# Kernel optimization log

Hardware: AMD Instinct MI355X
Metric: run time of the kernel (lower is better)

Reference implementation:

```python
import jax, jax.numpy as jnp
import numpy as np

B, L = 1, 320
CS, CZ, CH, H, PQ, PV = 384, 128, 16, 12, 4, 8
INF, EPS = 1e5, 1e-8


def _quat_to_rot(q):
    w, x, y, z = q[..., 0], q[..., 1], q[..., 2], q[..., 3]
    r0 = jnp.stack([1 - 2*(y*y + z*z), 2*(x*y - w*z), 2*(x*z + w*y)], -1)
    r1 = jnp.stack([2*(x*y + w*z), 1 - 2*(x*x + z*z), 2*(y*z - w*x)], -1)
    r2 = jnp.stack([2*(x*z - w*y), 2*(y*z + w*x), 1 - 2*(x*x + y*y)], -1)
    return jnp.stack([r0, r1, r2], -2)


def setup_inputs():
    key = jax.random.key(0)
    ks = jax.random.split(key, 12)

    def lin(k, fan_in, fan_out):
        k1, k2 = jax.random.split(k)
        lim = 1.0 / np.sqrt(fan_in)
        return (jax.random.uniform(k1, (fan_in, fan_out), minval=-lim, maxval=lim, dtype=jnp.float32),
                jax.random.uniform(k2, (fan_out,), minval=-lim, maxval=lim, dtype=jnp.float32))

    s = jax.random.normal(ks[0], (B, L, CS), dtype=jnp.float32)
    quat = jax.random.normal(ks[1], (B, L, 4), dtype=jnp.float32)
    quat = quat / jnp.linalg.norm(quat, axis=-1, keepdims=True)
    rot = _quat_to_rot(quat)                                   # proper rotations (B,L,3,3)
    trans = 10.0 * jax.random.normal(ks[2], (B, L, 3), dtype=jnp.float32)
    z = jax.random.normal(ks[3], (B, L, L, CZ), dtype=jnp.float32)
    frame_mask = jnp.ones((B, L), dtype=jnp.float32)

    Wq, bq = lin(ks[4], CS, CH * H)
    Wkv, bkv = lin(ks[5], CS, 2 * CH * H)
    Wqp, bqp = lin(ks[6], CS, 6 * H * PQ)
    Wkvp, bkvp = lin(ks[7], CS, 6 * H * (PQ + PV))
    Wg, bg = lin(ks[8], CS, H * PQ)
    geom_weights = jnp.ones((3,), jnp.float32)
    dir_weight = jnp.asarray(0.5, jnp.float32)
    head_weights = 0.02 * jax.random.normal(ks[9], (H,), dtype=jnp.float32)
    concat_dim = H * (CH + 7 * PV) + H * CZ                    # 2400
    Wo, bo = lin(ks[10], concat_dim, CS)
    return dict(s=s, rot=rot, trans=trans, z=z, frame_mask=frame_mask,
                Wq=Wq, bq=bq, Wkv=Wkv, bkv=bkv, Wqp=Wqp, bqp=bqp,
                Wkvp=Wkvp, bkvp=bkvp, Wg=Wg, bg=bg,
                geom_weights=geom_weights, dir_weight=dir_weight,
                head_weights=head_weights, Wo=Wo, bo=bo)


def reference(s, rot, trans, z, frame_mask, Wq, bq, Wkv, bkv, Wqp, bqp,
              Wkvp, bkvp, Wg, bg, geom_weights, dir_weight, head_weights, Wo, bo):
    def proc_pts(pts_flat, P):
        # (B,L,6*H*P) -> rotate coords+translate, rotate dirs -> (B,L,H,P,6)
        pts = pts_flat.reshape(B, L, H, P, 6)
        coords = jnp.einsum('blij,blhpj->blhpi', rot, pts[..., :3]) + trans[:, :, None, None, :]
        dirs = jnp.einsum('blij,blhpj->blhpi', rot, pts[..., 3:])
        return jnp.concatenate([coords, dirs], -1)

    q = (s @ Wq + bq).reshape(B, L, H, CH)
    kv = s @ Wkv + bkv
    k = kv[..., :CH * H].reshape(B, L, H, CH)
    v = kv[..., CH * H:].reshape(B, L, H, CH)

    q_pts = proc_pts(s @ Wqp + bqp, PQ)
    kv_pts = s @ Wkvp + bkvp
    k_pts = proc_pts(kv_pts[..., :6 * H * PQ], PQ)
    v_pts = proc_pts(kv_pts[..., 6 * H * PQ:], PV)

    gate = jax.nn.sigmoid(s @ Wg + bg).reshape(B, L, H, PQ, 1)
    q_pts = q_pts * gate

    scalar_att = jnp.einsum('bqhc,bkhc->bhqk', q, k) / np.sqrt(CH).astype(np.float32)

    # position attention: per-pair point distances + log + inverse, mean over points
    delta = q_pts[:, :, None, :, :, :3] - k_pts[:, None, :, :, :, :3]   # (B,Lq,Lk,H,PQ,3)
    d = jnp.linalg.norm(delta, axis=-1)
    pos_att = (d + jnp.log(d + EPS) + 1.0 / (d + EPS)).mean(-1).transpose(0, 3, 1, 2)

    # direction attention: per-point dot minus cross-product 'curvature'
    qd, kd = q_pts[..., 3:], k_pts[..., 3:]
    dot = jnp.einsum('bqhpd,bkhpd->bqkhp', qd, kd)                       # (B,Lq,Lk,H,P)
    cr = jnp.cross(qd[:, :, None, :, None, :, :], kd[:, None, :, :, :, None, :])  # (B,Lq,Lk,H,Pk,Pq,3)
    cross = jnp.linalg.norm(cr, axis=-1).mean(-1)                        # (B,Lq,Lk,H,Pk)
    nq = jnp.linalg.norm(qd, axis=-1)[:, :, None]                        # (B,Lq,1,H,P)
    nk = jnp.linalg.norm(kd, axis=-1)[:, None]                           # (B,1,Lk,H,P)
    dir_att = (dot - cross / (nq * nk + EPS)).mean(-1).transpose(0, 3, 1, 2)

    att = scalar_att + dir_weight * (geom_weights[0] * pos_att + geom_weights[1] * dir_att)
    att = att * head_weights[:, None, None]
    mask2d = frame_mask[:, None, None, :] * frame_mask[:, None, :, None]  # (B,1,L,L)
    att = jax.nn.softmax(att + INF * (mask2d - 1.0), axis=-1)

    o_scalar = jnp.einsum('bhqk,bkhc->bqhc', att, v)
    o_geom = jnp.einsum('bhqk,bkhpd->bqhpd', att, v_pts)                 # (B,L,H,PV,6)

    # map aggregated geometry back into local frames
    rotT = jnp.swapaxes(rot, -1, -2)
    trans_inv = -jnp.einsum('blij,blj->bli', rotT, trans)
    lc = jnp.einsum('blij,blhpj->blhpi', rotT, o_geom[..., :3]) + trans_inv[:, :, None, None, :]
    ld = jnp.einsum('blij,blhpj->blhpi', rotT, o_geom[..., 3:6])
    ld = ld / jnp.maximum(jnp.linalg.norm(ld, axis=-1, keepdims=True), 1e-12)  # F.normalize
    ln = jnp.linalg.norm(lc, axis=-1, keepdims=True)
    o_geom7 = jnp.concatenate([lc, ld, ln], -1)                          # (B,L,H,PV,7)

    o_pair = jnp.einsum('bhij,bijk->bihk', att, z)                       # (B,L,H,CZ)
    out = jnp.concatenate([o_scalar.reshape(B, L, H * CH),
                           o_geom7.reshape(B, L, H * PV * 7),
                           o_pair.reshape(B, L, H * CZ)], -1)
    return out @ Wo + bo
```

## Files before the change

kernel.cpp:

```cpp
#include <hip/hip_runtime.h>
#include <hip/hip_bf16.h>
#include <math.h>

#define LSEQ 320
#define CS 384
#define CZ 128
#define CH 16
#define NH 12
#define PQ 4
#define PV 8
#define EPSF 1e-8f

typedef short short8 __attribute__((ext_vector_type(8)));
typedef float f32x4 __attribute__((ext_vector_type(4)));

__device__ __forceinline__ unsigned short f2b(float x) {
    union { float f; unsigned u; } v; v.f = x;
    unsigned r = (v.u + 0x7FFF + ((v.u >> 16) & 1)) >> 16;
    return (unsigned short)r;
}
__device__ __forceinline__ float b2f(unsigned short h) {
    union { unsigned u; float f; } v; v.u = ((unsigned)h) << 16;
    return v.f;
}

#define OFF_Q      0
#define OFF_KV     61440
#define OFF_QPT    184320
#define OFF_KPT    276480
#define OFF_OG     368640
#define OFF_ATTHI  552960
#define OFF_ATTLO  1372160
#define OFF_CCHI   2191360
#define OFF_CCLO   2575360
#define OFF_SHI    2959360
#define OFF_SLO    2990080
#define OFF_WCATHI 3020800
#define OFF_WCATLO 3361792
#define OFF_BCAT   3702784
#define OFF_WOHI   3704560
#define OFF_WOLO   4165360
#define OFF_VKVHI  4626160
#define OFF_VKVLO  4749040
#define OFF_QPR    4871920
#define OFF_KVPR   4964080
#define OFF_GATE   5240560

__global__ __launch_bounds__(256) void k_cast(
    const float* __restrict__ s,
    const float* __restrict__ Wq, const float* __restrict__ bq,
    const float* __restrict__ Wkv, const float* __restrict__ bkv,
    const float* __restrict__ Wqp, const float* __restrict__ bqp,
    const float* __restrict__ Wkvp, const float* __restrict__ bkvp,
    const float* __restrict__ Wg, const float* __restrict__ bg,
    const float* __restrict__ Wo,
    unsigned short* __restrict__ s_hi, unsigned short* __restrict__ s_lo,
    unsigned short* __restrict__ wcat_hi, unsigned short* __restrict__ wcat_lo,
    float* __restrict__ bcat,
    unsigned short* __restrict__ wo_hi, unsigned short* __restrict__ wo_lo)
{
    int i = blockIdx.x * 256 + threadIdx.x;
    if (i < 122880) {
        float x = s[i];
        unsigned short hi = f2b(x);
        s_hi[i] = hi; s_lo[i] = f2b(x - b2f(hi));
        return;
    }
    i -= 122880;
    if (i < 681984) {
        int k = i / 1776, c = i - k * 1776;
        float v;
        if (c < 192)       v = Wq[(size_t)k * 192 + c];
        else if (c < 576)  v = Wkv[(size_t)k * 384 + c - 192];
        else if (c < 864)  v = Wqp[(size_t)k * 288 + c - 576];
        else if (c < 1728) v = Wkvp[(size_t)k * 864 + c - 864];
        else               v = Wg[(size_t)k * 48 + c - 1728];
        unsigned short hi = f2b(v);
        wcat_hi[i] = hi; wcat_lo[i] = f2b(v - b2f(hi));
        return;
    }
    i -= 681984;
    if (i < 1776) {
        float v;
        if (i < 192)       v = bq[i];
        else if (i < 576)  v = bkv[i - 192];
        else if (i < 864)  v = bqp[i - 576];
        else if (i < 1728) v = bkvp[i - 864];
        else               v = bg[i - 1728];
        bcat[i] = v;
        return;
    }
    i -= 1776;
    if (i < 921600) {
        float v = Wo[i];
        unsigned short hi = f2b(v);
        wo_hi[i] = hi; wo_lo[i] = f2b(v - b2f(hi));
    }
}

__global__ __launch_bounds__(256) void k_proj(
    const unsigned short* __restrict__ s_hi, const unsigned short* __restrict__ s_lo,
    const unsigned short* __restrict__ wcat_hi, const unsigned short* __restrict__ wcat_lo,
    const float* __restrict__ bcat,
    float* __restrict__ qo, float* __restrict__ kvo,
    float* __restrict__ qpr, float* __restrict__ kvpr, float* __restrict__ gate)
{
    __shared__ unsigned short a_hi[64][56];
    __shared__ unsigned short a_lo[64][56];
    __shared__ unsigned short w_hi[48][56];
    __shared__ unsigned short w_lo[48][56];
    int col0 = blockIdx.x * 48, l0 = blockIdx.y * 64;
    int tid = threadIdx.x;
    int lane = tid & 63, w = tid >> 6;
    int ncol = lane & 15, blk = lane >> 4, mrow = (lane >> 4) * 4;

    float* dst; int nc, cbase; bool sig = false;
    if (col0 < 192)       { nc = 192; cbase = col0;        dst = qo;   }
    else if (col0 < 576)  { nc = 384; cbase = col0 - 192;  dst = kvo;  }
    else if (col0 < 864)  { nc = 288; cbase = col0 - 576;  dst = qpr;  }
    else if (col0 < 1728) { nc = 864; cbase = col0 - 864;  dst = kvpr; }
    else                  { nc = 48;  cbase = 0;           dst = gate; sig = true; }

    f32x4 acc[3] = {};
    for (int k0 = 0; k0 < 384; k0 += 32) {
        __syncthreads();
        {
            int row = tid >> 2, seg = tid & 3;
            size_t off = (size_t)(l0 + row) * 384 + k0 + seg * 8;
            *(short8*)&a_hi[row][seg * 8] = *(const short8*)(s_hi + off);
            *(short8*)&a_lo[row][seg * 8] = *(const short8*)(s_lo + off);
        }
        if (tid < 96) {
            int kk = tid / 3, coff = (tid % 3) * 16;
            size_t off = (size_t)(k0 + kk) * 1776 + col0 + coff;
            short8 h0 = *(const short8*)(wcat_hi + off);
            short8 h1 = *(const short8*)(wcat_hi + off + 8);
            short8 l0v = *(const short8*)(wcat_lo + off);
            short8 l1v = *(const short8*)(wcat_lo + off + 8);
            #pragma unroll
            for (int i = 0; i < 8; i++) {
                w_hi[coff + i][kk]     = (unsigned short)h0[i];
                w_hi[coff + 8 + i][kk] = (unsigned short)h1[i];
                w_lo[coff + i][kk]     = (unsigned short)l0v[i];
                w_lo[coff + 8 + i][kk] = (unsigned short)l1v[i];
            }
        }
        __syncthreads();
        short8 afh = *(short8*)&a_hi[w * 16 + ncol][blk * 8];
        short8 afl = *(short8*)&a_lo[w * 16 + ncol][blk * 8];
        #pragma unroll
        for (int s3 = 0; s3 < 3; s3++) {
            short8 bfh = *(short8*)&w_hi[s3 * 16 + ncol][blk * 8];
            short8 bfl = *(short8*)&w_lo[s3 * 16 + ncol][blk * 8];
            acc[s3] = __builtin_amdgcn_mfma_f32_16x16x32_bf16(afh, bfh, acc[s3], 0, 0, 0);
            acc[s3] = __builtin_amdgcn_mfma_f32_16x16x32_bf16(afh, bfl, acc[s3], 0, 0, 0);
            acc[s3] = __builtin_amdgcn_mfma_f32_16x16x32_bf16(afl, bfh, acc[s3], 0, 0, 0);
        }
    }
    #pragma unroll
    for (int s3 = 0; s3 < 3; s3++) {
        float bv = bcat[col0 + s3 * 16 + ncol];
        int cloc = cbase + s3 * 16 + ncol;
        #pragma unroll
        for (int r = 0; r < 4; r++) {
            float v2 = acc[s3][r] + bv;
            if (sig) v2 = 1.0f / (1.0f + expf(-v2));
            dst[(size_t)(l0 + w * 16 + mrow + r) * nc + cloc] = v2;
        }
    }
}

__global__ __launch_bounds__(256) void k_points(
    const float* __restrict__ qpr, const float* __restrict__ kvpr, const float* __restrict__ gate,
    const float* __restrict__ rot, const float* __restrict__ trans,
    const float* __restrict__ kv,
    float* __restrict__ qpt, float* __restrict__ kpt,
    unsigned short* __restrict__ vkv_hi, unsigned short* __restrict__ vkv_lo)
{
    __shared__ float vsh[96][6];
    int l = blockIdx.x, t = threadIdx.x;
    const float* R = rot + l * 9;
    float tx = trans[l * 3], ty = trans[l * 3 + 1], tz = trans[l * 3 + 2];
    if (t < 192) {
        const float* src; float g = 1.0f; float* dst = nullptr; int vj = -1;
        if (t < 48)      { src = qpr + (size_t)l * 288 + t * 6; g = gate[l * 48 + t]; dst = qpt + ((size_t)l * 48 + t) * 6; }
        else if (t < 96) { int j = t - 48; src = kvpr + (size_t)l * 864 + j * 6; dst = kpt + ((size_t)l * 48 + j) * 6; }
        else             { int j = t - 96; src = kvpr + (size_t)l * 864 + 288 + j * 6; vj = j; }
        float px = src[0], py = src[1], pz = src[2], ux = src[3], uy = src[4], uz = src[5];
        float c0 = R[0] * px + R[1] * py + R[2] * pz + tx;
        float c1 = R[3] * px + R[4] * py + R[5] * pz + ty;
        float c2 = R[6] * px + R[7] * py + R[8] * pz + tz;
        float d0 = R[0] * ux + R[1] * uy + R[2] * uz;
        float d1 = R[3] * ux + R[4] * uy + R[5] * uz;
        float d2 = R[6] * ux + R[7] * uy + R[8] * uz;
        if (vj >= 0) {
            vsh[vj][0] = c0; vsh[vj][1] = c1; vsh[vj][2] = c2;
            vsh[vj][3] = d0; vsh[vj][4] = d1; vsh[vj][5] = d2;
        } else {
            dst[0] = c0 * g; dst[1] = c1 * g; dst[2] = c2 * g;
            dst[3] = d0 * g; dst[4] = d1 * g; dst[5] = d2 * g;
        }
    }
    __syncthreads();
    #pragma unroll
    for (int e = 0; e < 3; e++) {
        int u = t * 3 + e;
        int h = u >> 6, n = u & 63;
        float val;
        if (n < 16) val = kv[(size_t)l * 384 + 192 + h * 16 + n];
        else        val = vsh[h * 8 + (n - 16) / 6][(n - 16) % 6];
        unsigned short hi = f2b(val);
        size_t idx = ((size_t)h * 64 + n) * 320 + l;
        vkv_hi[idx] = hi;
        vkv_lo[idx] = f2b(val - b2f(hi));
    }
}

__global__ __launch_bounds__(256) void k_att(
    const float* __restrict__ qb, const float* __restrict__ kvb,
    const float* __restrict__ qpt, const float* __restrict__ kpt,
    const float* __restrict__ fm, const float* __restrict__ gw,
    const float* __restrict__ dwp, const float* __restrict__ hwp,
    unsigned short* __restrict__ att_hi, unsigned short* __restrict__ att_lo)
{
    __shared__ float kp_sh[320][25];
    int tid = threadIdx.x;
    int w = tid >> 6, lane = tid & 63;
    int iq = blockIdx.x * 4 + w;
    int h = blockIdx.y;

    for (int idx = tid; idx < 7680; idx += 256) {
        int kk = idx / 24, j = idx - kk * 24;
        kp_sh[kk][j] = kpt[(size_t)kk * 288 + h * 24 + j];
    }
    __syncthreads();

    float qv[CH];
    #pragma unroll
    for (int c = 0; c < CH; c++) qv[c] = qb[(size_t)iq * 192 + h * CH + c];
    float qp[24];
    #pragma unroll
    for (int j = 0; j < 24; j++) qp[j] = qpt[(size_t)iq * 288 + h * 24 + j];
    float nq[PQ];
    #pragma unroll
    for (int p = 0; p < PQ; p++) {
        float x = qp[p * 6 + 3], y = qp[p * 6 + 4], zz = qp[p * 6 + 5];
        nq[p] = sqrtf(x * x + y * y + zz * zz);
    }
    float dwv = dwp[0], g0 = gw[0], g1 = gw[1], hwv = hwp[h];
    float fmi = fm[iq];

    float lg[5];
    #pragma unroll
    for (int r = 0; r < 5; r++) {
        int kk = r * 64 + lane;
        const float* kp = &kp_sh[kk][0];

        float scalar = 0.f;
        #pragma unroll
        for (int c = 0; c < CH; c++) scalar += qv[c] * kvb[(size_t)kk * 384 + h * CH + c];
        scalar *= 0.25f;

        float pos = 0.f;
        #pragma unroll
        for (int p = 0; p < PQ; p++) {
            float dx = qp[p * 6] - kp[p * 6], dy = qp[p * 6 + 1] - kp[p * 6 + 1], dz = qp[p * 6 + 2] - kp[p * 6 + 2];
            float d = sqrtf(dx * dx + dy * dy + dz * dz);
            pos += d + logf(d + EPSF) + 1.0f / (d + EPSF);
        }
        pos *= 0.25f;

        float dir = 0.f;
        #pragma unroll
        for (int p = 0; p < PQ; p++) {
            float kx = kp[p * 6 + 3], ky = kp[p * 6 + 4], kz = kp[p * 6 + 5];
            float nk = sqrtf(kx * kx + ky * ky + kz * kz);
            float cm = 0.f;
            #pragma unroll
            for (int pq = 0; pq < PQ; pq++) {
                float qx = qp[pq * 6 + 3], qy = qp[pq * 6 + 4], qz = qp[pq * 6 + 5];
                float cx = qy * kz - qz * ky;
                float cy = qz * kx - qx * kz;
                float cz = qx * ky - qy * kx;
                cm += sqrtf(cx * cx + cy * cy + cz * cz);
            }
            cm *= 0.25f;
            float qx = qp[p * 6 + 3], qy = qp[p * 6 + 4], qz = qp[p * 6 + 5];
            float dotp = qx * kx + qy * ky + qz * kz;
            dir += dotp - cm / (nq[p] * nk + EPSF);
        }
        dir *= 0.25f;

        float logit = scalar + dwv * (g0 * pos + g1 * dir);
        logit *= hwv;
        logit += 100000.0f * (fmi * fm[kk] - 1.0f);
        lg[r] = logit;
    }

    float mx = lg[0];
    #pragma unroll
    for (int r = 1; r < 5; r++) mx = fmaxf(mx, lg[r]);
    for (int m = 32; m; m >>= 1) mx = fmaxf(mx, __shfl_xor(mx, m, 64));

    float e[5], sm = 0.f;
    #pragma unroll
    for (int r = 0; r < 5; r++) { e[r] = expf(lg[r] - mx); sm += e[r]; }
    for (int m = 32; m; m >>= 1) sm += __shfl_xor(sm, m, 64);
    float inv = 1.0f / sm;
    #pragma unroll
    for (int r = 0; r < 5; r++) {
        float p = e[r] * inv;
        unsigned short hi = f2b(p);
        size_t idx = ((size_t)h * 320 + iq) * 320 + r * 64 + lane;
        att_hi[idx] = hi;
        att_lo[idx] = f2b(p - b2f(hi));
    }
}

__global__ __launch_bounds__(256) void k_initzero(
    const float* __restrict__ bo, float* __restrict__ out,
    float* __restrict__ ph_hi, float* __restrict__ ph_lo)
{
    int i = blockIdx.x * 256 + threadIdx.x;
    if (i < 204800) ph_hi[i] = 0.0f;
    else if (i < 409600) ph_lo[i - 204800] = 0.0f;
    else { int j = i - 409600; out[j] = bo[j % CS]; }
}

__global__ __launch_bounds__(64) void k_sv(
    const unsigned short* __restrict__ att_hi, const unsigned short* __restrict__ att_lo,
    const unsigned short* __restrict__ vkv_hi, const unsigned short* __restrict__ vkv_lo,
    unsigned short* __restrict__ cc_hi, unsigned short* __restrict__ cc_lo,
    float* __restrict__ og)
{
    __shared__ unsigned short a_hi[16][56];
    __shared__ unsigned short a_lo[16][56];
    __shared__ unsigned short bt_hi[64][56];
    __shared__ unsigned short bt_lo[64][56];
    int iq0 = blockIdx.x * 16, h = blockIdx.y;
    int tid = threadIdx.x;
    int ncol = tid & 15, blk = tid >> 4, mrow = (tid >> 4) * 4;

    f32x4 acc[4] = {};
    for (int k0 = 0; k0 < 320; k0 += 32) {
        __syncthreads();
        {
            int row = tid >> 2, seg = tid & 3;
            size_t off = ((size_t)h * 320 + iq0 + row) * 320 + k0 + seg * 8;
            *(short8*)&a_hi[row][seg * 8] = *(const short8*)(att_hi + off);
            *(short8*)&a_lo[row][seg * 8] = *(const short8*)(att_lo + off);
        }
        {
            size_t off = ((size_t)h * 64 + tid) * 320 + k0;
            #pragma unroll
            for (int j2 = 0; j2 < 4; j2++) {
                *(short8*)&bt_hi[tid][j2 * 8] = *(const short8*)(vkv_hi + off + j2 * 8);
                *(short8*)&bt_lo[tid][j2 * 8] = *(const short8*)(vkv_lo + off + j2 * 8);
            }
        }
        __syncthreads();
        short8 afh = *(short8*)&a_hi[ncol][blk * 8];
        short8 afl = *(short8*)&a_lo[ncol][blk * 8];
        #pragma unroll
        for (int s4 = 0; s4 < 4; s4++) {
            short8 bfh = *(short8*)&bt_hi[s4 * 16 + ncol][blk * 8];
            short8 bfl = *(short8*)&bt_lo[s4 * 16 + ncol][blk * 8];
            acc[s4] = __builtin_amdgcn_mfma_f32_16x16x32_bf16(afh, bfh, acc[s4], 0, 0, 0);
            acc[s4] = __builtin_amdgcn_mfma_f32_16x16x32_bf16(afh, bfl, acc[s4], 0, 0, 0);
            acc[s4] = __builtin_amdgcn_mfma_f32_16x16x32_bf16(afl, bfh, acc[s4], 0, 0, 0);
        }
    }
    #pragma unroll
    for (int s4 = 0; s4 < 4; s4++) {
        int n = s4 * 16 + ncol;
        #pragma unroll
        for (int r = 0; r < 4; r++) {
            int iq = iq0 + mrow + r;
            float v = acc[s4][r];
            if (n < 16) {
                unsigned short hi = f2b(v);
                size_t idx = (size_t)iq * 2400 + h * 16 + n;
                cc_hi[idx] = hi;
                cc_lo[idx] = f2b(v - b2f(hi));
            } else {
                og[(size_t)iq * 576 + h * 48 + (n - 16)] = v;
            }
        }
    }
}

__global__ __launch_bounds__(256) void k_pair(
    const unsigned short* __restrict__ att_hi, const float* __restrict__ z,
    unsigned short* __restrict__ cc_hi, unsigned short* __restrict__ cc_lo)
{
    __shared__ unsigned short a_sh[16][56];
    __shared__ unsigned short zt_sh[128][56];
    int iq = blockIdx.x;
    int tid = threadIdx.x;
    int lane = tid & 63, w = tid >> 6;
    int ncol = lane & 15, blk = lane >> 4, mrow = (lane >> 4) * 4;

    f32x4 acc[2] = {};
    for (int k0 = 0; k0 < 320; k0 += 32) {
        __syncthreads();
        if (tid < 64) {
            int row = tid >> 2, seg = tid & 3;
            *(short8*)&a_sh[row][seg * 8] =
                *(const short8*)(att_hi + (size_t)row * 102400 + (size_t)iq * 320 + k0 + seg * 8);
        }
        {
            int kk = tid >> 3, cb = (tid & 7) * 16;
            const float* src = z + ((size_t)iq * 320 + k0 + kk) * 128 + cb;
            #pragma unroll
            for (int g4 = 0; g4 < 4; g4++) {
                float4 f = *(const float4*)(src + g4 * 4);
                zt_sh[cb + g4 * 4 + 0][kk] = f2b(f.x);
                zt_sh[cb + g4 * 4 + 1][kk] = f2b(f.y);
                zt_sh[cb + g4 * 4 + 2][kk] = f2b(f.z);
                zt_sh[cb + g4 * 4 + 3][kk] = f2b(f.w);
            }
        }
        __syncthreads();
        short8 af = *(short8*)&a_sh[ncol][blk * 8];
        #pragma unroll
        for (int s2 = 0; s2 < 2; s2++) {
            short8 bf = *(short8*)&zt_sh[w * 32 + s2 * 16 + ncol][blk * 8];
            acc[s2] = __builtin_amdgcn_mfma_f32_16x16x32_bf16(af, bf, acc[s2], 0, 0, 0);
        }
    }
    #pragma unroll
    for (int s2 = 0; s2 < 2; s2++) {
        int n = w * 32 + s2 * 16 + ncol;
        #pragma unroll
        for (int r = 0; r < 4; r++) {
            int h = mrow + r;
            if (h < 12) {
                float v = acc[s2][r];
                unsigned short hi = f2b(v);
                size_t idx = (size_t)iq * 2400 + 864 + h * 128 + n;
                cc_hi[idx] = hi;
                cc_lo[idx] = f2b(v - b2f(hi));
            }
        }
    }
}

__global__ __launch_bounds__(96) void k_finish(
    const float* __restrict__ og, const float* __restrict__ rot, const float* __restrict__ trans,
    unsigned short* __restrict__ cc_hi, unsigned short* __restrict__ cc_lo)
{
    int iq = blockIdx.x, tid = threadIdx.x;
    int h = tid / PV, p = tid % PV;
    const float* R = rot + iq * 9;
    float tx = trans[iq * 3], ty = trans[iq * 3 + 1], tz = trans[iq * 3 + 2];
    const float* o = og + (size_t)iq * 576 + h * 48 + p * 6;
    float gx = o[0] - tx, gy = o[1] - ty, gz = o[2] - tz;
    float l0 = R[0] * gx + R[3] * gy + R[6] * gz;
    float l1 = R[1] * gx + R[4] * gy + R[7] * gz;
    float l2 = R[2] * gx + R[5] * gy + R[8] * gz;
    float dx = o[3], dy = o[4], dz = o[5];
    float e0 = R[0] * dx + R[3] * dy + R[6] * dz;
    float e1 = R[1] * dx + R[4] * dy + R[7] * dz;
    float e2 = R[2] * dx + R[5] * dy + R[8] * dz;
    float n = sqrtf(e0 * e0 + e1 * e1 + e2 * e2);
    float inv = 1.0f / fmaxf(n, 1e-12f);
    float ln = sqrtf(l0 * l0 + l1 * l1 + l2 * l2);
    float vals[7] = { l0, l1, l2, e0 * inv, e1 * inv, e2 * inv, ln };
    size_t base = (size_t)iq * 2400 + 192 + (h * PV + p) * 7;
    #pragma unroll
    for (int j = 0; j < 7; j++) {
        unsigned short hi = f2b(vals[j]);
        cc_hi[base + j] = hi;
        cc_lo[base + j] = f2b(vals[j] - b2f(hi));
    }
}

__global__ __launch_bounds__(256) void k_gemm(
    const unsigned short* __restrict__ cc_hi, const unsigned short* __restrict__ cc_lo,
    const unsigned short* __restrict__ wo_hi, const unsigned short* __restrict__ wo_lo,
    float* __restrict__ out)
{
    __shared__ unsigned short a_hi[64][56];
    __shared__ unsigned short a_lo[64][56];
    __shared__ unsigned short w_hi[48][56];
    __shared__ unsigned short w_lo[48][56];
    int iq0 = blockIdx.x * 64, col0 = blockIdx.y * 48, ks = blockIdx.z;
    int tid = threadIdx.x;
    int lane = tid & 63, w = tid >> 6;
    int ncol = lane & 15, blk = lane >> 4, mrow = (lane >> 4) * 4;

    f32x4 acc[3] = {};
    for (int kc = 0; kc < 15; kc++) {
        int k0 = ks * 480 + kc * 32;
        __syncthreads();
        {
            int row = tid >> 2, seg = tid & 3;
            size_t off = (size_t)(iq0 + row) * 2400 + k0 + seg * 8;
            *(short8*)&a_hi[row][seg * 8] = *(const short8*)(cc_hi + off);
            *(short8*)&a_lo[row][seg * 8] = *(const short8*)(cc_lo + off);
        }
        if (tid < 96) {
            int kk = tid / 3, coff = (tid % 3) * 16;
            size_t off = (size_t)(k0 + kk) * 384 + col0 + coff;
            short8 h0 = *(const short8*)(wo_hi + off);
            short8 h1 = *(const short8*)(wo_hi + off + 8);
            short8 l0v = *(const short8*)(wo_lo + off);
            short8 l1v = *(const short8*)(wo_lo + off + 8);
            #pragma unroll
            for (int i = 0; i < 8; i++) {
                w_hi[coff + i][kk]     = (unsigned short)h0[i];
                w_hi[coff + 8 + i][kk] = (unsigned short)h1[i];
                w_lo[coff + i][kk]     = (unsigned short)l0v[i];
                w_lo[coff + 8 + i][kk] = (unsigned short)l1v[i];
            }
        }
        __syncthreads();
        short8 afh = *(short8*)&a_hi[w * 16 + ncol][blk * 8];
        short8 afl = *(short8*)&a_lo[w * 16 + ncol][blk * 8];
        #pragma unroll
        for (int s3 = 0; s3 < 3; s3++) {
            short8 bfh = *(short8*)&w_hi[s3 * 16 + ncol][blk * 8];
            short8 bfl = *(short8*)&w_lo[s3 * 16 + ncol][blk * 8];
            acc[s3] = __builtin_amdgcn_mfma_f32_16x16x32_bf16(afh, bfh, acc[s3], 0, 0, 0);
            acc[s3] = __builtin_amdgcn_mfma_f32_16x16x32_bf16(afh, bfl, acc[s3], 0, 0, 0);
            acc[s3] = __builtin_amdgcn_mfma_f32_16x16x32_bf16(afl, bfh, acc[s3], 0, 0, 0);
        }
    }
    #pragma unroll
    for (int s3 = 0; s3 < 3; s3++) {
        int cn = col0 + s3 * 16 + ncol;
        #pragma unroll
        for (int r = 0; r < 4; r++)
            atomicAdd(&out[(size_t)(iq0 + w * 16 + mrow + r) * CS + cn], acc[s3][r]);
    }
}

extern "C" void kernel_launch(void* const* d_in, const int* in_sizes, int n_in,
                              void* d_out, int out_size, void* d_ws, size_t ws_size,
                              hipStream_t stream)
{
    const float* s     = (const float*)d_in[0];
    const float* rot   = (const float*)d_in[1];
    const float* trans = (const float*)d_in[2];
    const float* z     = (const float*)d_in[3];
    const float* fm    = (const float*)d_in[4];
    const float* Wq    = (const float*)d_in[5];
    const float* bq    = (const float*)d_in[6];
    const float* Wkv   = (const float*)d_in[7];
    const float* bkv   = (const float*)d_in[8];
    const float* Wqp   = (const float*)d_in[9];
    const float* bqp   = (const float*)d_in[10];
    const float* Wkvp  = (const float*)d_in[11];
    const float* bkvp  = (const float*)d_in[12];
    const float* Wg    = (const float*)d_in[13];
    const float* bg    = (const float*)d_in[14];
    const float* gw    = (const float*)d_in[15];
    const float* dw    = (const float*)d_in[16];
    const float* hw    = (const float*)d_in[17];
    const float* Wo    = (const float*)d_in[18];
    const float* bo    = (const float*)d_in[19];

    float* ws = (float*)d_ws;
    float*          q       = ws + OFF_Q;
    float*          kv      = ws + OFF_KV;
    float*          qpt     = ws + OFF_QPT;
    float*          kpt     = ws + OFF_KPT;
    float*          og      = ws + OFF_OG;
    unsigned short* att_hi  = (unsigned short*)(ws + OFF_ATTHI);
    unsigned short* att_lo  = (unsigned short*)(ws + OFF_ATTLO);
    float*          ph_hi   = ws + OFF_ATTHI + 12 * 51200;
    float*          ph_lo   = ws + OFF_ATTLO + 12 * 51200;
    unsigned short* cc_hi   = (unsigned short*)(ws + OFF_CCHI);
    unsigned short* cc_lo   = (unsigned short*)(ws + OFF_CCLO);
    unsigned short* s_hi    = (unsigned short*)(ws + OFF_SHI);
    unsigned short* s_lo    = (unsigned short*)(ws + OFF_SLO);
    unsigned short* wcat_hi = (unsigned short*)(ws + OFF_WCATHI);
    unsigned short* wcat_lo = (unsigned short*)(ws + OFF_WCATLO);
    float*          bcat    = ws + OFF_BCAT;
    unsigned short* wo_hi   = (unsigned short*)(ws + OFF_WOHI);
    unsigned short* wo_lo   = (unsigned short*)(ws + OFF_WOLO);
    unsigned short* vkv_hi  = (unsigned short*)(ws + OFF_VKVHI);
    unsigned short* vkv_lo  = (unsigned short*)(ws + OFF_VKVLO);
    float*          qpr     = ws + OFF_QPR;
    float*          kvpr    = ws + OFF_KVPR;
    float*          gate    = ws + OFF_GATE;
    float* out = (float*)d_out;

    k_cast<<<dim3(6752), dim3(256), 0, stream>>>(s, Wq, bq, Wkv, bkv, Wqp, bqp,
                                                 Wkvp, bkvp, Wg, bg, Wo,
                                                 s_hi, s_lo, wcat_hi, wcat_lo, bcat,
                                                 wo_hi, wo_lo);
    k_proj<<<dim3(37, 5), dim3(256), 0, stream>>>(s_hi, s_lo, wcat_hi, wcat_lo, bcat,
                                                  q, kv, qpr, kvpr, gate);
    k_points<<<dim3(LSEQ), dim3(256), 0, stream>>>(qpr, kvpr, gate, rot, trans, kv,
                                                   qpt, kpt, vkv_hi, vkv_lo);
    k_att<<<dim3(80, NH), dim3(256), 0, stream>>>(q, kv, qpt, kpt, fm, gw, dw, hw,
                                                  att_hi, att_lo);
    k_initzero<<<dim3(2080), dim3(256), 0, stream>>>(bo, out, ph_hi, ph_lo);
    k_sv<<<dim3(20, NH), dim3(64), 0, stream>>>(att_hi, att_lo, vkv_hi, vkv_lo,
                                                cc_hi, cc_lo, og);
    k_pair<<<dim3(LSEQ), dim3(256), 0, stream>>>(att_hi, z, cc_hi, cc_lo);
    k_finish<<<dim3(LSEQ), dim3(96), 0, stream>>>(og, rot, trans, cc_hi, cc_lo);
    k_gemm<<<dim3(5, 8, 5), dim3(256), 0, stream>>>(cc_hi, cc_lo, wo_hi, wo_lo, out);
}
```

Measured before the change: 223.9 us.

## Fuse finish into sv, fold zeroing into cast, split-K reduce, add bf16x3 precision

Several changes land together. The frame back-transform kernel is merged into k_sv through a shared-memory staging buffer, and the partial-buffer zeroing moves into k_cast, which removes two launches. The output GEMM now writes split-K partials that a new k_reduce kernel sums with the bias, replacing atomics. In k_att, K points, K scalar features and precomputed key-direction norms are staged in LDS, the cross-product norm is computed through the Lagrange identity, and fast intrinsics are used. Accuracy also goes up: k_proj uses a three-way bf16 split with six MFMAs, and k_pair adds the low attention term. Both add compute and memory traffic.

```diff
diff --git a/kernel.cpp b/kernel.cpp
--- a/kernel.cpp
+++ b/kernel.cpp
@@ -24,27 +24,30 @@
     return v.f;
 }
 
-#define OFF_Q      0
-#define OFF_KV     61440
-#define OFF_QPT    184320
-#define OFF_KPT    276480
-#define OFF_OG     368640
-#define OFF_ATTHI  552960
-#define OFF_ATTLO  1372160
-#define OFF_CCHI   2191360
-#define OFF_CCLO   2575360
-#define OFF_SHI    2959360
-#define OFF_SLO    2990080
-#define OFF_WCATHI 3020800
-#define OFF_WCATLO 3361792
-#define OFF_BCAT   3702784
-#define OFF_WOHI   3704560
-#define OFF_WOLO   4165360
-#define OFF_VKVHI  4626160
-#define OFF_VKVLO  4749040
-#define OFF_QPR    4871920
-#define OFF_KVPR   4964080
-#define OFF_GATE   5240560
+#define OFF_Q       0
+#define OFF_KV      61440
+#define OFF_QPT     184320
+#define OFF_KPT     276480
+#define OFF_KNRM    368640
+#define OFF_ATTHI   552960
+#define OFF_ATTLO   1372160
+#define OFF_CCHI    2191360
+#define OFF_CCLO    2575360
+#define OFF_SHI     2959360
+#define OFF_SMID    2990080
+#define OFF_SLO     3020800
+#define OFF_WCATHI  3051520
+#define OFF_WCATMID 3392512
+#define OFF_WCATLO  3733504
+#define OFF_BCAT    4074496
+#define OFF_WOHI    4076272
+#define OFF_WOLO    4537072
+#define OFF_VKVHI   4997872
+#define OFF_VKVLO   5120752
+#define OFF_QPR     5243632
+#define OFF_KVPR    5335792
+#define OFF_GATE    5612272
+#define OFF_PART    5627632
 
 __global__ __launch_bounds__(256) void k_cast(
     const float* __restrict__ s,
@@ -54,16 +57,21 @@
     const float* __restrict__ Wkvp, const float* __restrict__ bkvp,
     const float* __restrict__ Wg, const float* __restrict__ bg,
     const float* __restrict__ Wo,
-    unsigned short* __restrict__ s_hi, unsigned short* __restrict__ s_lo,
-    unsigned short* __restrict__ wcat_hi, unsigned short* __restrict__ wcat_lo,
+    unsigned short* __restrict__ s_hi, unsigned short* __restrict__ s_mid,
+    unsigned short* __restrict__ s_lo,
+    unsigned short* __restrict__ w_hi, unsigned short* __restrict__ w_mid,
+    unsigned short* __restrict__ w_lo,
     float* __restrict__ bcat,
-    unsigned short* __restrict__ wo_hi, unsigned short* __restrict__ wo_lo)
+    unsigned short* __restrict__ wo_hi, unsigned short* __restrict__ wo_lo,
+    float* __restrict__ ph_hi, float* __restrict__ ph_lo)
 {
     int i = blockIdx.x * 256 + threadIdx.x;
     if (i < 122880) {
         float x = s[i];
         unsigned short hi = f2b(x);
-        s_hi[i] = hi; s_lo[i] = f2b(x - b2f(hi));
+        float r1 = x - b2f(hi);
+        unsigned short mid = f2b(r1);
+        s_hi[i] = hi; s_mid[i] = mid; s_lo[i] = f2b(r1 - b2f(mid));
         return;
     }
     i -= 122880;
@@ -76,7 +84,9 @@
         else if (c < 1728) v = Wkvp[(size_t)k * 864 + c - 864];
         else               v = Wg[(size_t)k * 48 + c - 1728];
         unsigned short hi = f2b(v);
-        wcat_hi[i] = hi; wcat_lo[i] = f2b(v - b2f(hi));
+        float r1 = v - b2f(hi);
+        unsigned short mid = f2b(r1);
+        w_hi[i] = hi; w_mid[i] = mid; w_lo[i] = f2b(r1 - b2f(mid));
         return;
     }
     i -= 681984;
@@ -95,20 +105,25 @@
         float v = Wo[i];
         unsigned short hi = f2b(v);
         wo_hi[i] = hi; wo_lo[i] = f2b(v - b2f(hi));
-    }
+        return;
+    }
+    i -= 921600;
+    if (i < 204800) { ph_hi[i] = 0.0f; return; }
+    i -= 204800;
+    if (i < 204800) ph_lo[i] = 0.0f;
 }
 
 __global__ __launch_bounds__(256) void k_proj(
-    const unsigned short* __restrict__ s_hi, const unsigned short* __restrict__ s_lo,
-    const unsigned short* __restrict__ wcat_hi, const unsigned short* __restrict__ wcat_lo,
+    const unsigned short* __restrict__ s_hi, const unsigned short* __restrict__ s_mid,
+    const unsigned short* __restrict__ s_lo,
+    const unsigned short* __restrict__ wc_hi, const unsigned short* __restrict__ wc_mid,
+    const unsigned short* __restrict__ wc_lo,
     const float* __restrict__ bcat,
     float* __restrict__ qo, float* __restrict__ kvo,
     float* __restrict__ qpr, float* __restrict__ kvpr, float* __restrict__ gate)
 {
-    __shared__ unsigned short a_hi[64][56];
-    __shared__ unsigned short a_lo[64][56];
-    __shared__ unsigned short w_hi[48][56];
-    __shared__ unsigned short w_lo[48][56];
+    __shared__ unsigned short a_h[64][56], a_m[64][56], a_l[64][56];
+    __shared__ unsigned short w_h[48][56], w_m[48][56], w_l[48][56];
     int col0 = blockIdx.x * 48, l0 = blockIdx.y * 64;
     int tid = threadIdx.x;
     int lane = tid & 63, w = tid >> 6;
@@ -127,34 +142,44 @@
         {
             int row = tid >> 2, seg = tid & 3;
             size_t off = (size_t)(l0 + row) * 384 + k0 + seg * 8;
-            *(short8*)&a_hi[row][seg * 8] = *(const short8*)(s_hi + off);
-            *(short8*)&a_lo[row][seg * 8] = *(const short8*)(s_lo + off);
+            *(short8*)&a_h[row][seg * 8] = *(const short8*)(s_hi + off);
+            *(short8*)&a_m[row][seg * 8] = *(const short8*)(s_mid + off);
+            *(short8*)&a_l[row][seg * 8] = *(const short8*)(s_lo + off);
         }
         if (tid < 96) {
             int kk = tid / 3, coff = (tid % 3) * 16;
             size_t off = (size_t)(k0 + kk) * 1776 + col0 + coff;
-            short8 h0 = *(const short8*)(wcat_hi + off);
-            short8 h1 = *(const short8*)(wcat_hi + off + 8);
-            short8 l0v = *(const short8*)(wcat_lo + off);
-            short8 l1v = *(const short8*)(wcat_lo + off + 8);
+            short8 h0 = *(const short8*)(wc_hi + off);
+            short8 h1 = *(const short8*)(wc_hi + off + 8);
+            short8 m0 = *(const short8*)(wc_mid + off);
+            short8 m1 = *(const short8*)(wc_mid + off + 8);
+            short8 l0v = *(const short8*)(wc_lo + off);
+            short8 l1v = *(const short8*)(wc_lo + off + 8);
             #pragma unroll
             for (int i = 0; i < 8; i++) {
-                w_hi[coff + i][kk]     = (unsigned short)h0[i];
-                w_hi[coff + 8 + i][kk] = (unsigned short)h1[i];
-                w_lo[coff + i][kk]     = (unsigned short)l0v[i];
-                w_lo[coff + 8 + i][kk] = (unsigned short)l1v[i];
-            }
-        }
-        __syncthreads();
-        short8 afh = *(short8*)&a_hi[w * 16 + ncol][blk * 8];
-        short8 afl = *(short8*)&a_lo[w * 16 + ncol][blk * 8];
+                w_h[coff + i][kk]     = (unsigned short)h0[i];
+                w_h[coff + 8 + i][kk] = (unsigned short)h1[i];
+                w_m[coff + i][kk]     = (unsigned short)m0[i];
+                w_m[coff + 8 + i][kk] = (unsigned short)m1[i];
+                w_l[coff + i][kk]     = (unsigned short)l0v[i];
+                w_l[coff + 8 + i][kk] = (unsigned short)l1v[i];
+            }
+        }
+        __syncthreads();
+        short8 afh = *(short8*)&a_h[w * 16 + ncol][blk * 8];
+        short8 afm = *(short8*)&a_m[w * 16 + ncol][blk * 8];
+        short8 afl = *(short8*)&a_l[w * 16 + ncol][blk * 8];
         #pragma unroll
         for (int s3 = 0; s3 < 3; s3++) {
-            short8 bfh = *(short8*)&w_hi[s3 * 16 + ncol][blk * 8];
-            short8 bfl = *(short8*)&w_lo[s3 * 16 + ncol][blk * 8];
-            acc[s3] = __builtin_amdgcn_mfma_f32_16x16x32_bf16(afh, bfh, acc[s3], 0, 0, 0);
+            short8 bfh = *(short8*)&w_h[s3 * 16 + ncol][blk * 8];
+            short8 bfm = *(short8*)&w_m[s3 * 16 + ncol][blk * 8];
+            short8 bfl = *(short8*)&w_l[s3 * 16 + ncol][blk * 8];
+            acc[s3] = __builtin_amdgcn_mfma_f32_16x16x32_bf16(afm, bfm, acc[s3], 0, 0, 0);
             acc[s3] = __builtin_amdgcn_mfma_f32_16x16x32_bf16(afh, bfl, acc[s3], 0, 0, 0);
             acc[s3] = __builtin_amdgcn_mfma_f32_16x16x32_bf16(afl, bfh, acc[s3], 0, 0, 0);
+            acc[s3] = __builtin_amdgcn_mfma_f32_16x16x32_bf16(afh, bfm, acc[s3], 0, 0, 0);
+            acc[s3] = __builtin_amdgcn_mfma_f32_16x16x32_bf16(afm, bfh, acc[s3], 0, 0, 0);
+            acc[s3] = __builtin_amdgcn_mfma_f32_16x16x32_bf16(afh, bfh, acc[s3], 0, 0, 0);
         }
     }
     #pragma unroll
@@ -174,7 +199,7 @@
     const float* __restrict__ qpr, const float* __restrict__ kvpr, const float* __restrict__ gate,
     const float* __restrict__ rot, const float* __restrict__ trans,
     const float* __restrict__ kv,
-    float* __restrict__ qpt, float* __restrict__ kpt,
+    float* __restrict__ qpt, float* __restrict__ kpt, float* __restrict__ knrm,
     unsigned short* __restrict__ vkv_hi, unsigned short* __restrict__ vkv_lo)
 {
     __shared__ float vsh[96][6];
@@ -199,6 +224,9 @@
         } else {
             dst[0] = c0 * g; dst[1] = c1 * g; dst[2] = c2 * g;
             dst[3] = d0 * g; dst[4] = d1 * g; dst[5] = d2 * g;
+            if (t >= 48) {
+                knrm[(size_t)(t - 48) * 320 + l] = sqrtf(d0 * d0 + d1 * d1 + d2 * d2);
+            }
         }
     }
     __syncthreads();
@@ -219,19 +247,24 @@
 __global__ __launch_bounds__(256) void k_att(
     const float* __restrict__ qb, const float* __restrict__ kvb,
     const float* __restrict__ qpt, const float* __restrict__ kpt,
+    const float* __restrict__ knrm,
     const float* __restrict__ fm, const float* __restrict__ gw,
     const float* __restrict__ dwp, const float* __restrict__ hwp,
     unsigned short* __restrict__ att_hi, unsigned short* __restrict__ att_lo)
 {
-    __shared__ float kp_sh[320][25];
+    __shared__ float kp_sh[320][45];
     int tid = threadIdx.x;
     int w = tid >> 6, lane = tid & 63;
     int iq = blockIdx.x * 4 + w;
     int h = blockIdx.y;
 
-    for (int idx = tid; idx < 7680; idx += 256) {
-        int kk = idx / 24, j = idx - kk * 24;
-        kp_sh[kk][j] = kpt[(size_t)kk * 288 + h * 24 + j];
+    for (int idx = tid; idx < 320 * 44; idx += 256) {
+        int kk = idx / 44, j = idx - kk * 44;
+        float v;
+        if (j < 24)      v = kpt[(size_t)kk * 288 + h * 24 + j];
+        else if (j < 40) v = kvb[(size_t)kk * 384 + h * 16 + (j - 24)];
+        else             v = knrm[(size_t)(h * 4 + (j - 40)) * 320 + kk];
+        kp_sh[kk][j] = v;
     }
     __syncthreads();
 
@@ -241,11 +274,12 @@
     float qp[24];
     #pragma unroll
     for (int j = 0; j < 24; j++) qp[j] = qpt[(size_t)iq * 288 + h * 24 + j];
-    float nq[PQ];
+    float nq[PQ], nq2[PQ];
     #pragma unroll
     for (int p = 0; p < PQ; p++) {
         float x = qp[p * 6 + 3], y = qp[p * 6 + 4], zz = qp[p * 6 + 5];
-        nq[p] = sqrtf(x * x + y * y + zz * zz);
+        nq2[p] = x * x + y * y + zz * zz;
+        nq[p] = sqrtf(nq2[p]);
     }
     float dwv = dwp[0], g0 = gw[0], g1 = gw[1], hwv = hwp[h];
     float fmi = fm[iq];
@@ -254,40 +288,40 @@
     #pragma unroll
     for (int r = 0; r < 5; r++) {
         int kk = r * 64 + lane;
-        const float* kp = &kp_sh[kk][0];
+        const float* row = &kp_sh[kk][0];
 
         float scalar = 0.f;
         #pragma unroll
-        for (int c = 0; c < CH; c++) scalar += qv[c] * kvb[(size_t)kk * 384 + h * CH + c];
+        for (int c = 0; c < CH; c++) scalar += qv[c] * row[24 + c];
         scalar *= 0.25f;
 
         float pos = 0.f;
         #pragma unroll
         for (int p = 0; p < PQ; p++) {
-            float dx = qp[p * 6] - kp[p * 6], dy = qp[p * 6 + 1] - kp[p * 6 + 1], dz = qp[p * 6 + 2] - kp[p * 6 + 2];
-            float d = sqrtf(dx * dx + dy * dy + dz * dz);
-            pos += d + logf(d + EPSF) + 1.0f / (d + EPSF);
+            float dx = qp[p * 6] - row[p * 6];
+            float dy = qp[p * 6 + 1] - row[p * 6 + 1];
+            float dz = qp[p * 6 + 2] - row[p * 6 + 2];
+            float d = __builtin_amdgcn_sqrtf(dx * dx + dy * dy + dz * dz);
+            float de = d + EPSF;
+            pos += d + __logf(de) + __builtin_amdgcn_rcpf(de);
         }
         pos *= 0.25f;
 
         float dir = 0.f;
         #pragma unroll
         for (int p = 0; p < PQ; p++) {
-            float kx = kp[p * 6 + 3], ky = kp[p * 6 + 4], kz = kp[p * 6 + 5];
-            float nk = sqrtf(kx * kx + ky * ky + kz * kz);
-            float cm = 0.f;
+            float kx = row[p * 6 + 3], ky = row[p * 6 + 4], kz = row[p * 6 + 5];
+            float nk = row[40 + p];
+            float nk2 = nk * nk;
+            float cm = 0.f, dself = 0.f;
             #pragma unroll
             for (int pq = 0; pq < PQ; pq++) {
-                float qx = qp[pq * 6 + 3], qy = qp[pq * 6 + 4], qz = qp[pq * 6 + 5];
-                float cx = qy * kz - qz * ky;
-                float cy = qz * kx - qx * kz;
-                float cz = qx * ky - qy * kx;
-                cm += sqrtf(cx * cx + cy * cy + cz * cz);
+                float dq = qp[pq * 6 + 3] * kx + qp[pq * 6 + 4] * ky + qp[pq * 6 + 5] * kz;
+                if (pq == p) dself = dq;
+                cm += __builtin_amdgcn_sqrtf(fmaxf(nq2[pq] * nk2 - dq * dq, 0.0f));
             }
             cm *= 0.25f;
-            float qx = qp[p * 6 + 3], qy = qp[p * 6 + 4], qz = qp[p * 6 + 5];
-            float dotp = qx * kx + qy * ky + qz * kz;
-            dir += dotp - cm / (nq[p] * nk + EPSF);
+            dir += dself - cm * __builtin_amdgcn_rcpf(nq[p] * nk + EPSF);
         }
         dir *= 0.25f;
 
@@ -304,7 +338,7 @@
 
     float e[5], sm = 0.f;
     #pragma unroll
-    for (int r = 0; r < 5; r++) { e[r] = expf(lg[r] - mx); sm += e[r]; }
+    for (int r = 0; r < 5; r++) { e[r] = __expf(lg[r] - mx); sm += e[r]; }
     for (int m = 32; m; m >>= 1) sm += __shfl_xor(sm, m, 64);
     float inv = 1.0f / sm;
     #pragma unroll
@@ -317,26 +351,17 @@
     }
 }
 
-__global__ __launch_bounds__(256) void k_initzero(
-    const float* __restrict__ bo, float* __restrict__ out,
-    float* __restrict__ ph_hi, float* __restrict__ ph_lo)
-{
-    int i = blockIdx.x * 256 + threadIdx.x;
-    if (i < 204800) ph_hi[i] = 0.0f;
-    else if (i < 409600) ph_lo[i - 204800] = 0.0f;
-    else { int j = i - 409600; out[j] = bo[j % CS]; }
-}
-
 __global__ __launch_bounds__(64) void k_sv(
     const unsigned short* __restrict__ att_hi, const unsigned short* __restrict__ att_lo,
     const unsigned short* __restrict__ vkv_hi, const unsigned short* __restrict__ vkv_lo,
-    unsigned short* __restrict__ cc_hi, unsigned short* __restrict__ cc_lo,
-    float* __restrict__ og)
+    const float* __restrict__ rot, const float* __restrict__ trans,
+    unsigned short* __restrict__ cc_hi, unsigned short* __restrict__ cc_lo)
 {
     __shared__ unsigned short a_hi[16][56];
     __shared__ unsigned short a_lo[16][56];
     __shared__ unsigned short bt_hi[64][56];
     __shared__ unsigned short bt_lo[64][56];
+    __shared__ float ogsh[16][49];
     int iq0 = blockIdx.x * 16, h = blockIdx.y;
     int tid = threadIdx.x;
     int ncol = tid & 15, blk = tid >> 4, mrow = (tid >> 4) * 4;
@@ -383,17 +408,47 @@
                 cc_hi[idx] = hi;
                 cc_lo[idx] = f2b(v - b2f(hi));
             } else {
-                og[(size_t)iq * 576 + h * 48 + (n - 16)] = v;
-            }
+                ogsh[mrow + r][n - 16] = v;
+            }
+        }
+    }
+    __syncthreads();
+    #pragma unroll
+    for (int t2 = tid; t2 < 128; t2 += 64) {
+        int iqr = t2 >> 3, p = t2 & 7;
+        int l = iq0 + iqr;
+        const float* R = rot + l * 9;
+        float tx = trans[l * 3], ty = trans[l * 3 + 1], tz = trans[l * 3 + 2];
+        const float* o = &ogsh[iqr][p * 6];
+        float gx = o[0] - tx, gy = o[1] - ty, gz = o[2] - tz;
+        float l0 = R[0] * gx + R[3] * gy + R[6] * gz;
+        float l1 = R[1] * gx + R[4] * gy + R[7] * gz;
+        float l2 = R[2] * gx + R[5] * gy + R[8] * gz;
+        float dx = o[3], dy = o[4], dz = o[5];
+        float e0 = R[0] * dx + R[3] * dy + R[6] * dz;
+        float e1 = R[1] * dx + R[4] * dy + R[7] * dz;
+        float e2 = R[2] * dx + R[5] * dy + R[8] * dz;
+        float n = sqrtf(e0 * e0 + e1 * e1 + e2 * e2);
+        float inv = 1.0f / fmaxf(n, 1e-12f);
+        float ln = sqrtf(l0 * l0 + l1 * l1 + l2 * l2);
+        float vals[7] = { l0, l1, l2, e0 * inv, e1 * inv, e2 * inv, ln };
+        size_t base = (size_t)l * 2400 + 192 + (h * PV + p) * 7;
+        #pragma unroll
+        for (int j = 0; j < 7; j++) {
+            unsigned short hi = f2b(vals[j]);
+            cc_hi[base + j] = hi;
+            cc_lo[base + j] = f2b(vals[j] - b2f(hi));
         }
     }
 }
 
 __global__ __launch_bounds__(256) void k_pair(
-    const unsigned short* __restrict__ att_hi, const float* __restrict__ z,
+    const unsigned short* __restrict__ att_hi, const unsigned short* __restrict__ att_lo,
+    const float* __restrict__ z,
     unsigned short* __restrict__ cc_hi, unsigned short* __restrict__ cc_lo)
 {
-    __shared__ unsigned short a_sh[16][56];
+    __shared__ unsigned short a_hi[16][56];
+    __shared__ unsigned short a_lo[16][56];
     __shared__ unsigned short zt_sh[128][56];
     int iq = blockIdx.x;
     int tid = threadIdx.x;
@@ -405,8 +460,9 @@
         __syncthreads();
         if (tid < 64) {
             int row = tid >> 2, seg = tid & 3;
-            *(short8*)&a_sh[row][seg * 8] =
-                *(const short8*)(att_hi + (size_t)row * 102400 + (size_t)iq * 320 + k0 + seg * 8);
+            size_t off = (size_t)row * 102400 + (size_t)iq * 320 + k0 + seg * 8;
+            *(short8*)&a_hi[row][seg * 8] = *(const short8*)(att_hi + off);
+            *(short8*)&a_lo[row][seg * 8] = *(const short8*)(att_lo + off);
         }
         {
             int kk = tid >> 3, cb = (tid & 7) * 16;
@@ -421,11 +477,13 @@
             }
         }
         __syncthreads();
-        short8 af = *(short8*)&a_sh[ncol][blk * 8];
+        short8 afh = *(short8*)&a_hi[ncol][blk * 8];
+        short8 afl = *(short8*)&a_lo[ncol][blk * 8];
         #pragma unroll
         for (int s2 = 0; s2 < 2; s2++) {
             short8 bf = *(short8*)&zt_sh[w * 32 + s2 * 16 + ncol][blk * 8];
-            acc[s2] = __builtin_amdgcn_mfma_f32_16x16x32_bf16(af, bf, acc[s2], 0, 0, 0);
+            acc[s2] = __builtin_amdgcn_mfma_f32_16x16x32_bf16(afl, bf, acc[s2], 0, 0, 0);
+            acc[s2] = __builtin_amdgcn_mfma_f32_16x16x32_bf16(afh, bf, acc[s2], 0, 0, 0);
         }
     }
     #pragma unroll
@@ -445,40 +503,10 @@
     }
 }
 
-__global__ __launch_bounds__(96) void k_finish(
-    const float* __restrict__ og, const float* __restrict__ rot, const float* __restrict__ trans,
-    unsigned short* __restrict__ cc_hi, unsigned short* __restrict__ cc_lo)
-{
-    int iq = blockIdx.x, tid = threadIdx.x;
-    int h = tid / PV, p = tid % PV;
-    const float* R = rot + iq * 9;
-    float tx = trans[iq * 3], ty = trans[iq * 3 + 1], tz = trans[iq * 3 + 2];
-    const float* o = og + (size_t)iq * 576 + h * 48 + p * 6;
-    float gx = o[0] - tx, gy = o[1] - ty, gz = o[2] - tz;
-    float l0 = R[0] * gx + R[3] * gy + R[6] * gz;
-    float l1 = R[1] * gx + R[4] * gy + R[7] * gz;
-    float l2 = R[2] * gx + R[5] * gy + R[8] * gz;
-    float dx = o[3], dy = o[4], dz = o[5];
-    float e0 = R[0] * dx + R[3] * dy + R[6] * dz;
-    float e1 = R[1] * dx + R[4] * dy + R[7] * dz;
-    float e2 = R[2] * dx + R[5] * dy + R[8] * dz;
-    float n = sqrtf(e0 * e0 + e1 * e1 + e2 * e2);
-    float inv = 1.0f / fmaxf(n, 1e-12f);
-    float ln = sqrtf(l0 * l0 + l1 * l1 + l2 * l2);
-    float vals[7] = { l0, l1, l2, e0 * inv, e1 * inv, e2 * inv, ln };
-    size_t base = (size_t)iq * 2400 + 192 + (h * PV + p) * 7;
-    #pragma unroll
-    for (int j = 0; j < 7; j++) {
-        unsigned short hi = f2b(vals[j]);
-        cc_hi[base + j] = hi;
-        cc_lo[base + j] = f2b(vals[j] - b2f(hi));
-    }
-}
-
 __global__ __launch_bounds__(256) void k_gemm(
     const unsigned short* __restrict__ cc_hi, const unsigned short* __restrict__ cc_lo,
     const unsigned short* __restrict__ wo_hi, const unsigned short* __restrict__ wo_lo,
-    float* __restrict__ out)
+    float* __restrict__ part)
 {
     __shared__ unsigned short a_hi[64][56];
     __shared__ unsigned short a_lo[64][56];
@@ -531,8 +559,18 @@
         int cn = col0 + s3 * 16 + ncol;
         #pragma unroll
         for (int r = 0; r < 4; r++)
-            atomicAdd(&out[(size_t)(iq0 + w * 16 + mrow + r) * CS + cn], acc[s3][r]);
-    }
+            part[((size_t)ks * 320 + iq0 + w * 16 + mrow + r) * 384 + cn] = acc[s3][r];
+    }
+}
+
+__global__ __launch_bounds__(256) void k_reduce(
+    const float* __restrict__ part, const float* __restrict__ bo, float* __restrict__ out)
+{
+    int i = blockIdx.x * 256 + threadIdx.x;
+    float v = bo[i % CS];
+    #pragma unroll
+    for (int ks = 0; ks < 5; ks++) v += part[(size_t)ks * 122880 + i];
+    out[i] = v;
 }
 
 extern "C" void kernel_launch(void* const* d_in, const int* in_sizes, int n_in,
@@ -565,7 +603,7 @@
     float*          kv      = ws + OFF_KV;
     float*          qpt     = ws + OFF_QPT;
     float*          kpt     = ws + OFF_KPT;
-    float*          og      = ws + OFF_OG;
+    float*          knrm    = ws + OFF_KNRM;
     unsigned short* att_hi  = (unsigned short*)(ws + OFF_ATTHI);
     unsigned short* att_lo  = (unsigned short*)(ws + OFF_ATTLO);
     float*          ph_hi   = ws + OFF_ATTHI + 12 * 51200;
@@ -573,9 +611,11 @@
     unsigned short* cc_hi   = (unsigned short*)(ws + OFF_CCHI);
     unsigned short* cc_lo   = (unsigned short*)(ws + OFF_CCLO);
     unsigned short* s_hi    = (unsigned short*)(ws + OFF_SHI);
+    unsigned short* s_mid   = (unsigned short*)(ws + OFF_SMID);
     unsigned short* s_lo    = (unsigned short*)(ws + OFF_SLO);
-    unsigned short* wcat_hi = (unsigned short*)(ws + OFF_WCATHI);
-    unsigned short* wcat_lo = (unsigned short*)(ws + OFF_WCATLO);
+    unsigned short* wc_hi   = (unsigned short*)(ws + OFF_WCATHI);
+    unsigned short* wc_mid  = (unsigned short*)(ws + OFF_WCATMID);
+    unsigned short* wc_lo   = (unsigned short*)(ws + OFF_WCATLO);
     float*          bcat    = ws + OFF_BCAT;
     unsigned short* wo_hi   = (unsigned short*)(ws + OFF_WOHI);
     unsigned short* wo_lo   = (unsigned short*)(ws + OFF_WOLO);
@@ -584,22 +624,22 @@
     float*          qpr     = ws + OFF_QPR;
     float*          kvpr    = ws + OFF_KVPR;
     float*          gate    = ws + OFF_GATE;
+    float*          part    = ws + OFF_PART;
     float* out = (float*)d_out;
 
-    k_cast<<<dim3(6752), dim3(256), 0, stream>>>(s, Wq, bq, Wkv, bkv, Wqp, bqp,
+    k_cast<<<dim3(8352), dim3(256), 0, stream>>>(s, Wq, bq, Wkv, bkv, Wqp, bqp,
                                                  Wkvp, bkvp, Wg, bg, Wo,
-                                                 s_hi, s_lo, wcat_hi, wcat_lo, bcat,
-                                                 wo_hi, wo_lo);
-    k_proj<<<dim3(37, 5), dim3(256), 0, stream>>>(s_hi, s_lo, wcat_hi, wcat_lo, bcat,
-                                                  q, kv, qpr, kvpr, gate);
+                                                 s_hi, s_mid, s_lo, wc_hi, wc_mid, wc_lo,
+                                                 bcat, wo_hi, wo_lo, ph_hi, ph_lo);
+    k_proj<<<dim3(37, 5), dim3(256), 0, stream>>>(s_hi, s_mid, s_lo, wc_hi, wc_mid, wc_lo,
+                                                  bcat, q, kv, qpr, kvpr, gate);
     k_points<<<dim3(LSEQ), dim3(256), 0, stream>>>(qpr, kvpr, gate, rot, trans, kv,
-                                                   qpt, kpt, vkv_hi, vkv_lo);
-    k_att<<<dim3(80, NH), dim3(256), 0, stream>>>(q, kv, qpt, kpt, fm, gw, dw, hw,
+                                                   qpt, kpt, knrm, vkv_hi, vkv_lo);
+    k_att<<<dim3(80, NH), dim3(256), 0, stream>>>(q, kv, qpt, kpt, knrm, fm, gw, dw, hw,
                                                   att_hi, att_lo);
-    k_initzero<<<dim3(2080), dim3(256), 0, stream>>>(bo, out, ph_hi, ph_lo);
     k_sv<<<dim3(20, NH), dim3(64), 0, stream>>>(att_hi, att_lo, vkv_hi, vkv_lo,
-                                                cc_hi, cc_lo, og);
-    k_pair<<<dim3(LSEQ), dim3(256), 0, stream>>>(att_hi, z, cc_hi, cc_lo);
-    k_finish<<<dim3(LSEQ), dim3(96), 0, stream>>>(og, rot, trans, cc_hi, cc_lo);
-    k_gemm<<<dim3(5, 8, 5), dim3(256), 0, stream>>>(cc_hi, cc_lo, wo_hi, wo_lo, out);
-}
+                                                rot, trans, cc_hi, cc_lo);
+    k_pair<<<dim3(LSEQ), dim3(256), 0, stream>>>(att_hi, att_lo, z, cc_hi, cc_lo);
+    k_gemm<<<dim3(5, 8, 5), dim3(256), 0, stream>>>(cc_hi, cc_lo, wo_hi, wo_lo, part);
+    k_reduce<<<dim3(480), dim3(256), 0, stream>>>(part, bo, out);
+}
```

Measured after the change: 234.1 us. 4.6% more time.
